# Optimization experiments

Measured on AMD Instinct MI355X. Metric: run time of the kernel, lower is better.

Reference implementation:

```python
import jax, jax.numpy as jnp
import numpy as np

T = 4096        # teams (HC nodes)
N_COORD = 3     # coordinators per team (OC, SC, DC)
N_POS = 32      # position coaches per coordinator
NPT = 1 + N_COORD + N_COORD * N_POS   # 100 nodes per team
N = T * NPT     # 409600 total nodes
IN_DIM = 128
EMB = 64


def _build_indices():
    base = np.arange(T, dtype=np.int32) * NPT
    hc_ids = base                                                    # [T]
    coord = base[:, None] + 1 + np.arange(N_COORD, dtype=np.int32)   # [T,3]
    pos = (base[:, None, None] + 1 + N_COORD
           + (np.arange(N_COORD, dtype=np.int32) * N_POS)[None, :, None]
           + np.arange(N_POS, dtype=np.int32)[None, None, :])        # [T,3,32]
    src1 = np.broadcast_to(coord[:, :, None], (T, N_COORD, N_POS)).reshape(-1)
    tgt1 = pos.reshape(-1)
    src2 = np.repeat(base, N_COORD)
    tgt2 = coord.reshape(-1)
    return (jnp.asarray(src1), jnp.asarray(tgt1),
            jnp.asarray(src2), jnp.asarray(tgt2), jnp.asarray(hc_ids))


def setup_inputs() -> dict:
    key = jax.random.key(0)
    k = jax.random.split(key, 5)
    src1, tgt1, src2, tgt2, hc_ids = _build_indices()
    gain = 1.414  # relu gain, xavier_normal-style scale
    f = jax.random.normal(k[0], (N, IN_DIM), jnp.float32)
    salary = jax.random.normal(k[1], (T, 1), jnp.float32)
    W_fc = jax.random.normal(k[2], (EMB, IN_DIM), jnp.float32) * gain * (2.0 / (IN_DIM + EMB)) ** 0.5
    W_attn = jax.random.normal(k[3], (1, 2 * EMB), jnp.float32) * gain * (2.0 / (2 * EMB + 1)) ** 0.5
    b_attn = jnp.zeros((1,), jnp.float32)
    W_out = jax.random.normal(k[4], (2, EMB + 1), jnp.float32) * gain * (2.0 / (EMB + 1 + 2)) ** 0.5
    b_out = jnp.zeros((2,), jnp.float32)
    return {"f": f, "salary": salary, "W_fc": W_fc, "W_attn": W_attn,
            "b_attn": b_attn, "W_out": W_out, "b_out": b_out,
            "src1": src1, "tgt1": tgt1, "src2": src2, "tgt2": tgt2,
            "hc_ids": hc_ids}


def _segment_softmax(e, seg, num_segments):
    m = jax.ops.segment_max(e, seg, num_segments=num_segments)
    ex = jnp.exp(e - m[seg])
    denom = jax.ops.segment_sum(ex, seg, num_segments=num_segments)
    return ex / denom[seg]


def _gat_level(z, src, tgt, W_attn, b_attn):
    # per-edge attention logit: leaky_relu(attn_fc([z_src, z_tgt]))
    z2 = jnp.concatenate([z[src], z[tgt]], axis=1)          # [E, 2*EMB]
    e = jax.nn.leaky_relu(z2 @ W_attn.T + b_attn)[:, 0]     # [E]
    alpha = _segment_softmax(e, src, N)                     # softmax over edges grouped by source
    agg = jax.ops.segment_sum(alpha[:, None] * z[tgt], src, num_segments=N)
    has_edge = jax.ops.segment_sum(jnp.ones_like(e), src, num_segments=N) > 0
    # only source nodes get their z replaced by relu(weighted sum)
    return jnp.where(has_edge[:, None], jax.nn.relu(agg), z)


def reference(f, salary, W_fc, W_attn, b_attn, W_out, b_out,
              src1, tgt1, src2, tgt2, hc_ids):
    z = jax.nn.relu(f @ W_fc.T)                             # [N, EMB]
    z = _gat_level(z, src1, tgt1, W_attn, b_attn)           # coord <- positions
    z = _gat_level(z, src2, tgt2, W_attn, b_attn)           # hc <- coords
    team_emb = z[hc_ids]                                    # [T, EMB]
    h = jnp.concatenate([team_emb, salary], axis=1)         # [T, EMB+1]
    y = jax.nn.relu(h @ W_out.T + b_out)                    # [T, 2]
    return jax.nn.softmax(y, axis=1)
```

## Files before the change

### kernel.cpp

```cpp
#include <hip/hip_runtime.h>

typedef short v8s __attribute__((ext_vector_type(8)));
typedef float v4f __attribute__((ext_vector_type(4)));
typedef unsigned int v4u __attribute__((ext_vector_type(4)));

#define NPT 100
#define IN_DIM 128

__device__ __forceinline__ unsigned int cvt_pk(float x0, float x1) {
    unsigned int r;
    asm("v_cvt_pk_bf16_f32 %0, %1, %2" : "=v"(r) : "v"(x0), "v"(x1));
    return r;
}
__device__ __forceinline__ float bflo(unsigned int u) { return __uint_as_float(u << 16); }
__device__ __forceinline__ float bfhi(unsigned int u) { return __uint_as_float(u & 0xffff0000u); }

union ABfrag { v8s v; v4u u; };

__device__ __forceinline__ ABfrag pack8(float4 x0, float4 x1) {
    ABfrag r;
    r.u[0] = cvt_pk(x0.x, x0.y);
    r.u[1] = cvt_pk(x0.z, x0.w);
    r.u[2] = cvt_pk(x1.x, x1.y);
    r.u[3] = cvt_pk(x1.z, x1.w);
    return r;
}

#define ISSUE(BUF, FP, T) do {                                                   \
    const float* rp_ = (FP) + rofs[T];                                           \
    _Pragma("unroll") for (int ks_ = 0; ks_ < 4; ++ks_) {                        \
        BUF[ks_][0] = *(const float4*)(rp_ + ks_ * 32);                          \
        BUF[ks_][1] = *(const float4*)(rp_ + ks_ * 32 + 4);                      \
    }                                                                            \
} while (0)

#define CONSUME(T, BUF) do {                                                     \
    v4f acc_[4] = {{0,0,0,0},{0,0,0,0},{0,0,0,0},{0,0,0,0}};                     \
    _Pragma("unroll") for (int ks_ = 0; ks_ < 4; ++ks_) {                        \
        ABfrag fr_ = pack8(BUF[ks_][0], BUF[ks_][1]);                            \
        _Pragma("unroll") for (int n_ = 0; n_ < 4; ++n_) {                       \
            v8s bh_ = *(const v8s*)&wl[(ks_ * 256 + n_ * 64 + lane) * 8];        \
            acc_[n_] = __builtin_amdgcn_mfma_f32_16x16x32_bf16(fr_.v, bh_, acc_[n_], 0, 0, 0); \
        }                                                                        \
    }                                                                            \
    float zr_[4][4];                                                             \
    _Pragma("unroll") for (int n_ = 0; n_ < 4; ++n_)                             \
        _Pragma("unroll") for (int j_ = 0; j_ < 4; ++j_)                         \
            zr_[n_][j_] = fmaxf(acc_[n_][j_], 0.f);                              \
    _Pragma("unroll") for (int n_ = 0; n_ < 4; ++n_) {                           \
        zp[T][n_][0] = cvt_pk(zr_[n_][0], zr_[n_][1]);                           \
        zp[T][n_][1] = cvt_pk(zr_[n_][2], zr_[n_][3]);                           \
    }                                                                            \
    const bool useL_ = ((T) == 0) && (g == 0);            \
    _Pragma("unroll") for (int j_ = 0; j_ < 4; ++j_) {                           \
        float d_ = (useL_ ? aLv[0] : aRv[0]) * zr_[0][j_]                        \
                 + (useL_ ? aLv[1] : aRv[1]) * zr_[1][j_]                        \
                 + (useL_ ? aLv[2] : aRv[2]) * zr_[2][j_]                        \
                 + (useL_ ? aLv[3] : aRv[3]) * zr_[3][j_];                       \
        d_ += __shfl_xor(d_, 8, 64); d_ += __shfl_xor(d_, 4, 64);                \
        d_ += __shfl_xor(d_, 2, 64); d_ += __shfl_xor(d_, 1, 64);                \
        const int r_ = 16 * (T) + 4 * g + j_;                                    \
        if (l15 == j_ && ((T) < 6 || r_ < NPT)) sDa[r_] = d_;                    \
    }                                                                            \
} while (0)

#define TAIL(TEAMI) do {                                                         \
    {                       \
        const int c_ = lane >> 5, p_ = lane & 31;                                \
        float e_ = sDa[1 + c_] + sDa[4 + 32 * c_ + p_] + bA;                     \
        e_ = e_ > 0.f ? e_ : 0.01f * e_;                                         \
        float mx_ = e_;                                                          \
        mx_ = fmaxf(mx_, __shfl_xor(mx_, 16, 64)); mx_ = fmaxf(mx_, __shfl_xor(mx_, 8, 64)); \
        mx_ = fmaxf(mx_, __shfl_xor(mx_, 4, 64));  mx_ = fmaxf(mx_, __shfl_xor(mx_, 2, 64)); \
        mx_ = fmaxf(mx_, __shfl_xor(mx_, 1, 64));                                \
        float ex_ = __expf(e_ - mx_), sm_ = ex_;                                 \
        sm_ += __shfl_xor(sm_, 16, 64); sm_ += __shfl_xor(sm_, 8, 64);           \
        sm_ += __shfl_xor(sm_, 4, 64);  sm_ += __shfl_xor(sm_, 2, 64);           \
        sm_ += __shfl_xor(sm_, 1, 64);                                           \
        sDa[4 + lane] = ex_ / sm_;                                               \
    }                                                                            \
    if (lane < 32) {                                                \
        float e_ = sDa[3] + sDa[68 + lane] + bA;                                 \
        e_ = e_ > 0.f ? e_ : 0.01f * e_;                                         \
        float mx_ = e_;                                                          \
        mx_ = fmaxf(mx_, __shfl_xor(mx_, 16, 64)); mx_ = fmaxf(mx_, __shfl_xor(mx_, 8, 64)); \
        mx_ = fmaxf(mx_, __shfl_xor(mx_, 4, 64));  mx_ = fmaxf(mx_, __shfl_xor(mx_, 2, 64)); \
        mx_ = fmaxf(mx_, __shfl_xor(mx_, 1, 64));                                \
        float ex_ = __expf(e_ - mx_), sm_ = ex_;                                 \
        sm_ += __shfl_xor(sm_, 16, 64); sm_ += __shfl_xor(sm_, 8, 64);           \
        sm_ += __shfl_xor(sm_, 4, 64);  sm_ += __shfl_xor(sm_, 2, 64);           \
        sm_ += __shfl_xor(sm_, 1, 64);                                           \
        sDa[68 + lane] = ex_ / sm_;                                              \
    }                                                                            \
     \
     \
    float zn_[3][4], sRn_[3];                                                    \
    _Pragma("unroll") for (int c_ = 0; c_ < 3; ++c_) {                           \
        float s_[4] = {0.f, 0.f, 0.f, 0.f};                                      \
        _Pragma("unroll") for (int ti_ = 0; ti_ < 3; ++ti_) {                    \
            const int T_ = 2 * c_ + ti_;                                         \
            float4 av_ = *(const float4*)&sDa[16 * T_ + 4 * g];                  \
            const float msk_ = (ti_ == 0) ? (g >= 1 ? 1.f : 0.f)                 \
                             : (ti_ == 2) ? (g == 0 ? 1.f : 0.f) : 1.f;          \
            av_.x *= msk_; av_.y *= msk_; av_.z *= msk_; av_.w *= msk_;          \
            _Pragma("unroll") for (int n_ = 0; n_ < 4; ++n_) {                   \
                s_[n_] += av_.x * bflo(zp[T_][n_][0]) + av_.y * bfhi(zp[T_][n_][0]) \
                        + av_.z * bflo(zp[T_][n_][1]) + av_.w * bfhi(zp[T_][n_][1]); \
            }                                                                    \
        }                                                                        \
        _Pragma("unroll") for (int n_ = 0; n_ < 4; ++n_) {                       \
            s_[n_] += __shfl_xor(s_[n_], 16, 64);                                \
            s_[n_] += __shfl_xor(s_[n_], 32, 64);                                \
            zn_[c_][n_] = fmaxf(s_[n_], 0.f);                                    \
        }                                                                        \
        float pr_ = aRv[0] * zn_[c_][0] + aRv[1] * zn_[c_][1]                    \
                  + aRv[2] * zn_[c_][2] + aRv[3] * zn_[c_][3];                   \
        pr_ += __shfl_xor(pr_, 8, 64); pr_ += __shfl_xor(pr_, 4, 64);            \
        pr_ += __shfl_xor(pr_, 2, 64); pr_ += __shfl_xor(pr_, 1, 64);            \
        sRn_[c_] = pr_;                                                          \
    }                                                                            \
    {                                                     \
        const float s0_ = sDa[0];                                                \
        float e0_ = s0_ + sRn_[0] + bA; e0_ = e0_ > 0.f ? e0_ : 0.01f * e0_;     \
        float e1_ = s0_ + sRn_[1] + bA; e1_ = e1_ > 0.f ? e1_ : 0.01f * e1_;     \
        float e2_ = s0_ + sRn_[2] + bA; e2_ = e2_ > 0.f ? e2_ : 0.01f * e2_;     \
        const float mx_ = fmaxf(e0_, fmaxf(e1_, e2_));                           \
        const float x0_ = __expf(e0_ - mx_), x1_ = __expf(e1_ - mx_), x2_ = __expf(e2_ - mx_); \
        const float inv_ = 1.f / (x0_ + x1_ + x2_);                              \
        float p0_ = 0.f, p1_ = 0.f;                                              \
        _Pragma("unroll") for (int n_ = 0; n_ < 4; ++n_) {                       \
            const float zh_ = fmaxf((x0_ * zn_[0][n_] + x1_ * zn_[1][n_]         \
                                   + x2_ * zn_[2][n_]) * inv_, 0.f);             \
            p0_ += W_out[n_ * 16 + l15] * zh_;                                   \
            p1_ += W_out[65 + n_ * 16 + l15] * zh_;                              \
        }                                                                        \
        p0_ += __shfl_xor(p0_, 8, 64); p0_ += __shfl_xor(p0_, 4, 64);            \
        p0_ += __shfl_xor(p0_, 2, 64); p0_ += __shfl_xor(p0_, 1, 64);            \
        p1_ += __shfl_xor(p1_, 8, 64); p1_ += __shfl_xor(p1_, 4, 64);            \
        p1_ += __shfl_xor(p1_, 2, 64); p1_ += __shfl_xor(p1_, 1, 64);            \
        if (lane == 0) {                                                         \
            const float sal_ = salary[TEAMI];                                    \
            float y0_ = fmaxf(p0_ + W_out[64]  * sal_ + b_out[0], 0.f);          \
            float y1_ = fmaxf(p1_ + W_out[129] * sal_ + b_out[1], 0.f);          \
            const float mm_ = fmaxf(y0_, y1_);                                   \
            const float q0_ = __expf(y0_ - mm_), q1_ = __expf(y1_ - mm_);        \
            const float is_ = 1.f / (q0_ + q1_);                                 \
            out[(TEAMI) * 2 + 0] = q0_ * is_;                                    \
            out[(TEAMI) * 2 + 1] = q1_ * is_;                                    \
        }                                                                        \
    }                                                                            \
} while (0)

#define TEAM_BODY(BA, BB, FCUR, FNXT, HASN, TEAMI) do {                          \
    unsigned int zp[7][4][2];                                                    \
    CONSUME(0, BA); ISSUE(BA, FCUR, 2);                                          \
    CONSUME(1, BB); ISSUE(BB, FCUR, 3);                                          \
    CONSUME(2, BA); ISSUE(BA, FCUR, 4);                                          \
    CONSUME(3, BB); ISSUE(BB, FCUR, 5);                                          \
    CONSUME(4, BA); ISSUE(BA, FCUR, 6);                                          \
    CONSUME(5, BB); if (HASN) ISSUE(BB, FNXT, 0);                                \
    CONSUME(6, BA); if (HASN) ISSUE(BA, FNXT, 1);                                \
    TAIL(TEAMI);                                                                 \
} while (0)

__global__ __launch_bounds__(256, 2) void wteam2_kernel(
    const float* __restrict__ f, const float* __restrict__ salary,
    const float* __restrict__ W_fc, const float* __restrict__ W_attn,
    const float* __restrict__ b_attn, const float* __restrict__ W_out,
    const float* __restrict__ b_out, float* __restrict__ out)
{
    __shared__ __align__(16) unsigned short wl[8192];
    __shared__ __align__(16) float sD_all[4][112];

    const int tid  = threadIdx.x;
    const int lane = tid & 63;
    const int wave = tid >> 6;
    const int l15  = lane & 15;
    const int g    = lane >> 4;
    float* sDa = sD_all[wave];

    #pragma unroll
    for (int i = 0; i < 4; ++i) {
        const int s = i * 256 + tid;
        const int ks = s >> 8, nt = (s >> 6) & 3, sl = s & 63;
        const float* src = W_fc + (nt * 16 + (sl & 15)) * IN_DIM + ks * 32 + 8 * (sl >> 4);
        ABfrag wv = pack8(*(const float4*)src, *(const float4*)(src + 4));
        *(v4u*)&wl[s * 8] = wv.u;
    }

    float aLv[4], aRv[4];
    #pragma unroll
    for (int n = 0; n < 4; ++n) {
        aLv[n] = W_attn[n * 16 + l15];
        aRv[n] = W_attn[64 + n * 16 + l15];
    }
    const float bA = b_attn[0];

    int rofs[7];
    #pragma unroll
    for (int T = 0; T < 7; ++T) {
        int r = 16 * T + l15;
        if (r > NPT - 1) r = NPT - 1;
        rofs[T] = r * IN_DIM + 8 * g;
    }

    const size_t team0 = ((size_t)blockIdx.x * 4 + wave) * 2;
    const float* f0 = f + team0 * (NPT * IN_DIM);
    const float* f1 = f0 + NPT * IN_DIM;

    __syncthreads();

    float4 bufA[4][2], bufB[4][2];
    ISSUE(bufA, f0, 0);
    ISSUE(bufB, f0, 1);

    TEAM_BODY(bufA, bufB, f0, f1, true,  team0);
    TEAM_BODY(bufB, bufA, f1, f1, false, team0 + 1);
}

extern "C" void kernel_launch(void* const* d_in, const int* in_sizes, int n_in,
                              void* d_out, int out_size, void* d_ws, size_t ws_size,
                              hipStream_t stream) {
    const float* f      = (const float*)d_in[0];
    const float* salary = (const float*)d_in[1];
    const float* W_fc   = (const float*)d_in[2];
    const float* W_attn = (const float*)d_in[3];
    const float* b_attn = (const float*)d_in[4];
    const float* W_out  = (const float*)d_in[5];
    const float* b_out  = (const float*)d_in[6];
    wteam2_kernel<<<dim3(512), dim3(256), 0, stream>>>(
        f, salary, W_fc, W_attn, b_attn, W_out, b_out, (float*)d_out);
}
```

Measured before the change: 44.06 us.

## Process one team per wave with single buffer and higher occupancy

```diff
diff --git a/kernel.cpp b/kernel.cpp
--- a/kernel.cpp
+++ b/kernel.cpp
@@ -27,7 +27,8 @@
 }
 
 #define ISSUE(BUF, FP, T) do {                                                   \
-    const float* rp_ = (FP) + rofs[T];                                           \
+    int r_ = 16 * (T) + l15; if (r_ > NPT - 1) r_ = NPT - 1;                     \
+    const float* rp_ = (FP) + r_ * IN_DIM + 8 * g;                               \
     _Pragma("unroll") for (int ks_ = 0; ks_ < 4; ++ks_) {                        \
         BUF[ks_][0] = *(const float4*)(rp_ + ks_ * 32);                          \
         BUF[ks_][1] = *(const float4*)(rp_ + ks_ * 32 + 4);                      \
@@ -151,19 +152,7 @@
     }                                                                            \
 } while (0)
 
-#define TEAM_BODY(BA, BB, FCUR, FNXT, HASN, TEAMI) do {                          \
-    unsigned int zp[7][4][2];                                                    \
-    CONSUME(0, BA); ISSUE(BA, FCUR, 2);                                          \
-    CONSUME(1, BB); ISSUE(BB, FCUR, 3);                                          \
-    CONSUME(2, BA); ISSUE(BA, FCUR, 4);                                          \
-    CONSUME(3, BB); ISSUE(BB, FCUR, 5);                                          \
-    CONSUME(4, BA); ISSUE(BA, FCUR, 6);                                          \
-    CONSUME(5, BB); if (HASN) ISSUE(BB, FNXT, 0);                                \
-    CONSUME(6, BA); if (HASN) ISSUE(BA, FNXT, 1);                                \
-    TAIL(TEAMI);                                                                 \
-} while (0)
-
-__global__ __launch_bounds__(256, 2) void wteam2_kernel(
+__global__ __launch_bounds__(256, 4) void wteam1_kernel(
     const float* __restrict__ f, const float* __restrict__ salary,
     const float* __restrict__ W_fc, const float* __restrict__ W_attn,
     const float* __restrict__ b_attn, const float* __restrict__ W_out,
@@ -196,26 +185,23 @@
     }
     const float bA = b_attn[0];
 
-    int rofs[7];
-    #pragma unroll
-    for (int T = 0; T < 7; ++T) {
-        int r = 16 * T + l15;
-        if (r > NPT - 1) r = NPT - 1;
-        rofs[T] = r * IN_DIM + 8 * g;
-    }
-
-    const size_t team0 = ((size_t)blockIdx.x * 4 + wave) * 2;
-    const float* f0 = f + team0 * (NPT * IN_DIM);
-    const float* f1 = f0 + NPT * IN_DIM;
+    const size_t team = (size_t)blockIdx.x * 4 + wave;
+    const float* f0 = f + team * (NPT * IN_DIM);
 
     __syncthreads();
 
-    float4 bufA[4][2], bufB[4][2];
-    ISSUE(bufA, f0, 0);
-    ISSUE(bufB, f0, 1);
-
-    TEAM_BODY(bufA, bufB, f0, f1, true,  team0);
-    TEAM_BODY(bufB, bufA, f1, f1, false, team0 + 1);
+    float4 buf[4][2];
+    unsigned int zp[7][4][2];
+
+    ISSUE(buf, f0, 0);
+    CONSUME(0, buf); ISSUE(buf, f0, 1);
+    CONSUME(1, buf); ISSUE(buf, f0, 2);
+    CONSUME(2, buf); ISSUE(buf, f0, 3);
+    CONSUME(3, buf); ISSUE(buf, f0, 4);
+    CONSUME(4, buf); ISSUE(buf, f0, 5);
+    CONSUME(5, buf); ISSUE(buf, f0, 6);
+    CONSUME(6, buf);
+    TAIL(team);
 }
 
 extern "C" void kernel_launch(void* const* d_in, const int* in_sizes, int n_in,
@@ -228,6 +214,6 @@
     const float* b_attn = (const float*)d_in[4];
     const float* W_out  = (const float*)d_in[5];
     const float* b_out  = (const float*)d_in[6];
-    wteam2_kernel<<<dim3(512), dim3(256), 0, stream>>>(
+    wteam1_kernel<<<dim3(1024), dim3(256), 0, stream>>>(
         f, salary, W_fc, W_attn, b_attn, W_out, b_out, (float*)d_out);
 }
```

Result: slower. 45.37 us (+3.0%).
